# Kernel optimization log

Measured on AMD Instinct MI355X. Metric: run time of the kernel, lower is better.

Reference implementation:

```python
import jax, jax.numpy as jnp
import numpy as np
from jax import lax

B, NF, NOBJ, SZ = 16, 4, 32, 128
HALF = SZ // 2  # 64


def _build_grid(h, w):
    ys = jnp.linspace(0.0, 1.0, h)
    xs = jnp.linspace(0.0, 1.0, w)
    gy, gx = jnp.meshgrid(ys, xs, indexing='ij')
    g = jnp.stack([gy, gx], axis=-1)  # (H, W, 2)
    return jnp.concatenate([g, 1.0 - g], axis=-1)[None]  # (1, H, W, 4)


def setup_inputs() -> dict:
    key = jax.random.key(0)
    ks = jax.random.split(key, 8)
    images = jax.random.normal(ks[0], (B, 3 * NF, SZ, SZ), dtype=jnp.float32)
    rois = jax.random.randint(ks[1], (B, NOBJ, SZ, SZ), 0, 2).astype(jnp.bool_)
    conv1_w = jax.random.normal(ks[2], (64, 3 * NF, 3, 3), dtype=jnp.float32) * 0.05
    conv1_b = jnp.zeros((64,), dtype=jnp.float32)
    conv2_w = jax.random.normal(ks[3], (128, 64, 3, 3), dtype=jnp.float32) * 0.05
    conv2_b = jnp.zeros((128,), dtype=jnp.float32)
    dense_w = jax.random.normal(ks[4], (128, 4), dtype=jnp.float32) * 0.1
    dense_b = jnp.zeros((128,), dtype=jnp.float32)
    return dict(images=images, rois=rois, conv1_w=conv1_w, conv1_b=conv1_b,
                conv2_w=conv2_w, conv2_b=conv2_b, dense_w=dense_w, dense_b=dense_b)


def _conv(x, w, b):
    y = lax.conv_general_dilated(x, w, window_strides=(1, 1), padding='SAME',
                                 dimension_numbers=('NCHW', 'OIHW', 'NCHW'))
    return y + b[None, :, None, None]


def reference(images, rois, conv1_w, conv1_b, conv2_w, conv2_b, dense_w, dense_b):
    # conv stack
    x = jax.nn.relu(_conv(images, conv1_w, conv1_b))
    x = lax.reduce_window(x, -jnp.inf, lax.max, (1, 1, 2, 2), (1, 1, 2, 2), 'VALID')
    x = jax.nn.relu(_conv(x, conv2_w, conv2_b))  # (B, 128, 64, 64)
    # soft position embed
    grid = _build_grid(HALF, HALF)  # (1, 64, 64, 4)
    pe = grid @ dense_w.T + dense_b  # (1, 64, 64, 128)
    x = x + jnp.transpose(pe, (0, 3, 1, 2))  # (B, 128, 64, 64)
    # roi pool: nearest-downsample masks 128->64 (indices 0,2,4,...)
    r = rois[:, :, ::2, ::2].astype(x.dtype)  # (B, O, 64, 64)
    masked = x[:, None] * r[:, :, None]  # (B, O, 128, 64, 64)
    return jnp.max(masked, axis=(-2, -1))  # (B, O, 128)
```

## Files before the change

### kernel.cpp

```cpp
#include <hip/hip_runtime.h>


typedef __attribute__((ext_vector_type(8))) short short8;
typedef __attribute__((ext_vector_type(4))) float f32x4;
typedef __attribute__((ext_vector_type(4))) unsigned short us4;
typedef __attribute__((ext_vector_type(2))) unsigned short u16x2;
typedef unsigned short u16;
typedef unsigned int u32;

__device__ __forceinline__ u16 f2bf(float f) {
  u32 u = __builtin_bit_cast(u32, f);
  return (u16)((u + 0x7fffu + ((u >> 16) & 1u)) >> 16);
}
__device__ __forceinline__ u32 pkmaxu(u32 a, u32 b) {
  u16x2 x = __builtin_bit_cast(u16x2, a), y = __builtin_bit_cast(u16x2, b);
  return __builtin_bit_cast(u32, __builtin_elementwise_max(x, y));
}
__device__ __forceinline__ u32 map2(u32 v) {
  u32 flip = ((v & 0x80008000u) >> 15) * 0xFFFFu;
  return v ^ (flip | 0x80008000u);
}
__device__ __forceinline__ float unmap1(u32 m) {
  u32 b = m ^ ((m & 0x8000u) ? 0x8000u : 0xFFFFu);
  return __builtin_bit_cast(float, b << 16);
}

namespace {

__global__ __launch_bounds__(256) void kiop(const float* __restrict__ img,
                                            u16* __restrict__ imgT,
                                            const unsigned* __restrict__ rois,
                                            unsigned* __restrict__ rmask,
                                            const float* __restrict__ w2,
                                            u16* __restrict__ Aw2,
                                            const float* __restrict__ w1,
                                            u16* __restrict__ Aw1) {
  __shared__ alignas(16) u16 ST[2048];
  const int bx = blockIdx.x;
  const int t = threadIdx.x;
  if (bx < 2048) {
    const int row = bx & 127, b = bx >> 7;
#pragma unroll
    for (int i = 0; i < 2; ++i) {
      const int e = i * 256 + t;
      ST[(e >> 2) * 16 + 12 + (e & 3)] = 0;
    }
#pragma unroll
    for (int i = 0; i < 6; ++i) {
      const int e = i * 256 + t;
      const int ci = e >> 7, col = e & 127;
      const float v = img[(((size_t)(b * 12 + ci)) << 14) + row * 128 + col];
      ST[col * 16 + ci] = f2bf(v);
    }
    __syncthreads();
    us4* dst = (us4*)(imgT + (((size_t)(b * 128 + row)) << 11));
#pragma unroll
    for (int i = 0; i < 2; ++i) {
      const int q = i * 256 + t;
      dst[q] = *(const us4*)&ST[q * 4];
    }
  } else if (bx < 2176) {
    const int lane = t & 63;
    u32 ok = 1u;
#pragma unroll
    for (int i = 0; i < 4; ++i) {
      u32 v = rois[lane * 4 + i];
      ok &= ((v <= 1u) || (v == 0x3f800000u)) ? 1u : 0u;
    }
    const bool isWord = (__all((int)ok) != 0);
    const unsigned char* roisB = (const unsigned char*)rois;
    const int pi = (bx - 2048) * 256 + t;
    const int b = pi >> 11;
    const int pp = pi & 2047;
    const int h = pp >> 5;
    const int wp = pp & 31;
    const size_t base = (size_t)b * 32 * 16384 + (size_t)(2 * h) * 128 + 4 * wp;
    u32 m0 = 0, m1 = 0;
#pragma unroll
    for (int o = 0; o < 32; ++o) {
      const size_t idx = base + (size_t)o * 16384;
      if (isWord) {
        const uint4 q = *(const uint4*)&rois[idx];
        m0 |= (u32)(q.x != 0u) << o;
        m1 |= (u32)(q.z != 0u) << o;
      } else {
        const u32 q = *(const u32*)&roisB[idx];
        m0 |= (u32)((q & 0xffu) != 0u) << o;
        m1 |= (u32)((q & 0xff0000u) != 0u) << o;
      }
    }
    *(uint2*)&rmask[b * 4096 + h * 64 + wp * 2] = make_uint2(m0, m1);
  } else if (bx < 2464) {
    const int idx = (bx - 2176) * 256 + t;
    const int j = idx & 7;
    const int lane = (idx >> 3) & 63;
    const int t3 = idx >> 9;
    const int ks = t3 % 18, cot = t3 / 18;
    const int m = lane & 15, g = lane >> 4;
    const int co = cot * 16 + m;
    const int k = ks * 32 + g * 8 + j;
    const int rc = k >> 6, ci = k & 63;
    Aw2[idx] = f2bf(w2[co * 576 + ci * 9 + rc]);
  } else {
    const int idx = (bx - 2464) * 256 + t;
    const int j = idx & 7;
    const int lane = (idx >> 3) & 63;
    const int t3 = idx >> 9;
    const int ks = t3 % 5, cot = t3 / 5;
    const int m = lane & 15, g = lane >> 4;
    const int co = cot * 16 + m;
    const int k = ks * 32 + g * 8 + j;
    const int rc = k >> 4, cip = k & 15;
    const float v = (rc < 9 && cip < 12) ? w1[co * 108 + cip * 9 + rc] : 0.f;
    Aw1[idx] = f2bf(v);
  }
}

__global__ __launch_bounds__(256) void k1_mfma(const u16* __restrict__ imgT,
                                               const u16* __restrict__ Aw1,
                                               const float* __restrict__ b1,
                                               u16* __restrict__ pooledT) {
  __shared__ alignas(16) u16 SIMG[8192];
  __shared__ alignas(16) u16 PT[64 * 68];
  const int h2 = blockIdx.x, b = blockIdx.y;
  const int t = threadIdx.x, wv = t >> 6, l = t & 63;

#pragma unroll
  for (int i = 0; i < 4; ++i) {
    const int q = i * 256 + t;
    const int sr = q >> 8, off = q & 255;
    const int irow = 2 * h2 - 1 + sr;
    short8 v = {0, 0, 0, 0, 0, 0, 0, 0};
    if ((unsigned)irow < 128u)
      v = *(const short8*)(imgT + (((size_t)(b * 128 + irow)) << 11) + off * 8);
    *(short8*)((char*)SIMG + ((q * 16) ^ (((q >> 3) & 1) << 4))) = v;
  }
  __syncthreads();

  const int m16 = l & 15, g = l >> 4;
  const int colhalf = wv >> 1, cotbase = (wv & 1) * 2;
  const int cipb = (g & 1) * 16;
  f32x4 acc[2][8];
#pragma unroll
  for (int ct = 0; ct < 2; ++ct)
#pragma unroll
    for (int pt = 0; pt < 8; ++pt) acc[ct][pt] = (f32x4){0.f, 0.f, 0.f, 0.f};

  const u16* awb = Aw1 + (size_t)l * 8;
  const short8 z8 = {0, 0, 0, 0, 0, 0, 0, 0};

#pragma unroll
  for (int ks = 0; ks < 5; ++ks) {
    short8 a0 = *(const short8*)(awb + (cotbase * 5 + ks) * 512);
    short8 a1 = *(const short8*)(awb + ((cotbase + 1) * 5 + ks) * 512);
    const bool pz = (ks == 4) && (g >= 2);
    const int rc = pz ? 0 : (2 * ks + (g >> 1));
    const int rr = (rc * 11) >> 5;
    const int cc = rc - rr * 3;
    const int d = m16 - 1 + cc;
    const int sb = (d < 0) ? 1 : ((d >> 2) & 1);
    const int base = rr * 4096 + d * 32 + colhalf * 2048 + (cipb ^ (sb << 4));
    const bool killLo = (cc == 0) && (m16 == 0) && (colhalf == 0);
    const bool killHi = (cc == 2) && (m16 == 15) && (colhalf == 1);
#pragma unroll
    for (int pt = 0; pt < 8; ++pt) {
      const int r01 = pt >> 2, ct2 = pt & 3;
      short8 bv = *(const short8*)((const char*)SIMG + base + r01 * 4096 + ct2 * 512);
      bool kill = pz;
      if (ct2 == 0) kill = kill || killLo;
      if (ct2 == 3) kill = kill || killHi;
      if (kill) bv = z8;
      acc[0][pt] = __builtin_amdgcn_mfma_f32_16x16x32_bf16(a0, bv, acc[0][pt], 0, 0, 0);
      acc[1][pt] = __builtin_amdgcn_mfma_f32_16x16x32_bf16(a1, bv, acc[1][pt], 0, 0, 0);
    }
  }

#pragma unroll
  for (int ct = 0; ct < 2; ++ct) {
    const int cot = cotbase + ct;
#pragma unroll
    for (int r = 0; r < 4; ++r) {
      const int co = cot * 16 + g * 4 + r;
      const float bias = b1[co];
#pragma unroll
      for (int ct2 = 0; ct2 < 4; ++ct2) {
        float v0 = fmaxf(acc[ct][ct2][r] + bias, 0.f);
        float v1 = fmaxf(acc[ct][4 + ct2][r] + bias, 0.f);
        float vv = fmaxf(v0, v1);
        vv = fmaxf(vv, __shfl_xor(vv, 1, 64));
        if (!(m16 & 1)) {
          const int pw = colhalf * 32 + ct2 * 8 + (m16 >> 1);
          PT[pw * 68 + co] = f2bf(vv);
        }
      }
    }
  }
  __syncthreads();
  u16* dst = pooledT + (((size_t)(b * 64 + h2)) << 12);
#pragma unroll
  for (int i = 0; i < 4; ++i) {
    const int e = (i * 256 + t) * 4;
    const int pw = e >> 6, co = e & 63;
    *(us4*)(dst + e) = *(const us4*)&PT[pw * 68 + co];
  }
}

__global__ __launch_bounds__(256) void k2f(const u16* __restrict__ pooledT,
                                           const u16* __restrict__ Aw,
                                           const float* __restrict__ b2,
                                           const float* __restrict__ dw,
                                           const float* __restrict__ db,
                                           const unsigned* __restrict__ rmask,
                                           u32* __restrict__ partial) {
  __shared__ alignas(16) char SB[32768];
  __shared__ u32 MS[128];
  const int hp = blockIdx.x, b = blockIdx.y;
  const int t = threadIdx.x, wv = t >> 6, l = t & 63;

#pragma unroll
  for (int i = 0; i < 8; ++i) {
    const int chunk = i * 4 + wv;
    const int row = chunk >> 3;
    const int hin = 2 * hp - 1 + row;
    short8 v = {0, 0, 0, 0, 0, 0, 0, 0};
    if ((unsigned)hin < 64u)
      v = *(const short8*)(pooledT + (((size_t)(b * 64 + hin)) << 12) +
                           ((chunk & 7) << 9) + l * 8);
    const int lin = chunk * 1024 + l * 16;
    *(short8*)(SB + (lin ^ (((lin >> 7) & 7) << 4))) = v;
  }
  if (t < 128) MS[t] = rmask[b * 4096 + hp * 128 + t];
  __syncthreads();

  const int m16 = l & 15, g = l >> 4;
  const int kbyte = g * 16;
  f32x4 acc[2][8];
#pragma unroll
  for (int ct = 0; ct < 2; ++ct)
#pragma unroll
    for (int n = 0; n < 8; ++n) acc[ct][n] = (f32x4){0.f, 0.f, 0.f, 0.f};

  const u16* aw0 = Aw + (size_t)wv * 36 * 512 + l * 8;
  const short8 z8 = {0, 0, 0, 0, 0, 0, 0, 0};

#pragma unroll
  for (int ks = 0; ks < 18; ++ks) {
    const int rc = ks >> 1, r = rc / 3, c = rc % 3;
    const int koff = r * 8192 + (ks & 1) * 64 + kbyte;
    short8 a0 = *(const short8*)(aw0 + ks * 512);
    short8 a1 = *(const short8*)(aw0 + (18 + ks) * 512);
    const int d = m16 + c - 1;
    const int base = (koff + d * 128) ^ ((d & 7) << 4);
    const bool edgeLo = (c == 0) && (m16 == 0);
    const bool edgeHi = (c == 2) && (m16 == 15);
#pragma unroll
    for (int n = 0; n < 8; ++n) {
      const int orw = n >> 2, n4 = n & 3;
      short8 bv = *(const short8*)(SB + base + orw * 8192 + n4 * 2048);
      if (c == 0 && n4 == 0) { if (edgeLo) bv = z8; }
      if (c == 2 && n4 == 3) { if (edgeHi) bv = z8; }
      acc[0][n] = __builtin_amdgcn_mfma_f32_16x16x32_bf16(a0, bv, acc[0][n], 0, 0, 0);
      acc[1][n] = __builtin_amdgcn_mfma_f32_16x16x32_bf16(a1, bv, acc[1][n], 0, 0, 0);
    }
  }

  __syncthreads();

  const float inv63 = 1.f / 63.f;
#pragma unroll
  for (int ct = 0; ct < 2; ++ct) {
    const int cot = wv * 2 + ct;
#pragma unroll
    for (int r2 = 0; r2 < 2; ++r2) {
      const int co0 = cot * 16 + g * 4 + r2 * 2;
      const float bias0 = b2[co0], bias1 = b2[co0 + 1];
      const float pA0 = dw[co0 * 4 + 0] - dw[co0 * 4 + 2];
      const float pB0 = dw[co0 * 4 + 1] - dw[co0 * 4 + 3];
      const float pC0 = dw[co0 * 4 + 2] + dw[co0 * 4 + 3] + db[co0];
      const float pA1 = dw[co0 * 4 + 4] - dw[co0 * 4 + 6];
      const float pB1 = dw[co0 * 4 + 5] - dw[co0 * 4 + 7];
      const float pC1 = dw[co0 * 4 + 6] + dw[co0 * 4 + 7] + db[co0 + 1];
#pragma unroll
      for (int orw = 0; orw < 2; ++orw) {
        const float gy = (float)(2 * hp + orw) * inv63;
        const float pe00 = gy * pA0 + pC0;
        const float pe01 = gy * pA1 + pC1;
#pragma unroll
        for (int n4 = 0; n4 < 4; ++n4) {
          const int w = n4 * 16 + m16;
          const int pos = orw * 64 + w;
          const float gx = (float)w * inv63;
          const float v0 = fmaxf(acc[ct][orw * 4 + n4][r2 * 2 + 0] + bias0, 0.f)
                           + pe00 + gx * pB0;
          const float v1 = fmaxf(acc[ct][orw * 4 + n4][r2 * 2 + 1] + bias1, 0.f)
                           + pe01 + gx * pB1;
          const u32 pk = map2((u32)f2bf(v0) | ((u32)f2bf(v1) << 16));
          *(u32*)(SB + ((pos * 256 + co0 * 2) ^ ((pos & 7) << 4))) = pk;
        }
      }
    }
  }
  __syncthreads();

  const int og = t >> 5, coq = t & 31;
  u32 a0[4], a1[4];
#pragma unroll
  for (int r = 0; r < 4; ++r) { a0[r] = 0x80008000u; a1[r] = 0x80008000u; }
  for (int pos = 0; pos < 128; ++pos) {
    const u32 mw = MS[pos];
    const uint2 x = *(const uint2*)(SB + ((pos * 256 + coq * 8) ^ ((pos & 7) << 4)));
#pragma unroll
    for (int r = 0; r < 4; ++r) {
      const int o = og * 4 + r;
      const u32 am = (u32)((int)(mw << (31 - o)) >> 31);
      a0[r] = pkmaxu(a0[r], x.x & am);
      a1[r] = pkmaxu(a1[r], x.y & am);
    }
  }
  u32* pslab = partial + (size_t)hp * 32768;
#pragma unroll
  for (int r = 0; r < 4; ++r) {
    const int o = og * 4 + r;
    *(uint2*)&pslab[((b * 32 + o) << 6) + coq * 2] = make_uint2(a0[r], a1[r]);
  }
}

__global__ __launch_bounds__(256) void k4_merge(const u32* __restrict__ partial,
                                                float* __restrict__ out) {
  const int idx = blockIdx.x * 256 + threadIdx.x;
  u32 v = partial[idx];
#pragma unroll
  for (int q = 1; q < 32; ++q) v = pkmaxu(v, partial[q * 32768 + idx]);
  float2 o2;
  o2.x = unmap1(v & 0xFFFFu);
  o2.y = unmap1(v >> 16);
  *(float2*)&out[idx * 2] = o2;
}

}

extern "C" void kernel_launch(void* const* d_in, const int* in_sizes, int n_in,
                              void* d_out, int out_size, void* d_ws, size_t ws_size,
                              hipStream_t stream) {
  const float* images = (const float*)d_in[0];
  const unsigned* rois = (const unsigned*)d_in[1];
  const float* w1 = (const float*)d_in[2];
  const float* b1 = (const float*)d_in[3];
  const float* w2 = (const float*)d_in[4];
  const float* b2 = (const float*)d_in[5];
  const float* dw = (const float*)d_in[6];
  const float* db = (const float*)d_in[7];
  float* out = (float*)d_out;

  char* ws = (char*)d_ws;
  unsigned* rmask = (unsigned*)(ws);
  u16* pooledT = (u16*)(ws + 0x40000);
  u16* Aw2 = (u16*)(ws + 0x840000);
  u16* Aw1 = (u16*)(ws + 0x864000);
  u16* imgT = (u16*)(ws + 0x900000);
  u32* partial = (u32*)(ws + 0xD00000);

  hipLaunchKernelGGL(kiop, dim3(2504), dim3(256), 0, stream,
                     images, imgT, rois, rmask, w2, Aw2, w1, Aw1);
  hipLaunchKernelGGL(k1_mfma, dim3(64, 16), dim3(256), 0, stream, imgT, Aw1, b1, pooledT);
  hipLaunchKernelGGL(k2f, dim3(32, 16), dim3(256), 0, stream,
                     pooledT, Aw2, b2, dw, db, rmask, partial);
  hipLaunchKernelGGL(k4_merge, dim3(128), dim3(256), 0, stream, partial, out);
}
```

Baseline: 61.64 us.

## Move roi-mask and conv2 weight prep into conv1 kernel; halve conv2 rows per block

The roi bitmask build and the conv2 weight repack move out of the first prep kernel and run as extra blocks of the conv1 MFMA kernel, which now uses a flat 1D grid. The aim is to overlap these side tasks with conv1 compute instead of serialising them before it. The conv2+pool kernel now covers one output row per block instead of two, doubling the grid to 1024 blocks and cutting LDS and accumulator registers for better occupancy. The cost is more halo reloads of pooled input and weight loads across blocks, plus 64 partial slabs for the merge kernel to reduce instead of 32.

```diff
diff --git a/kernel.cpp b/kernel.cpp
--- a/kernel.cpp
+++ b/kernel.cpp
@@ -29,10 +29,6 @@
 
 __global__ __launch_bounds__(256) void kiop(const float* __restrict__ img,
                                             u16* __restrict__ imgT,
-                                            const unsigned* __restrict__ rois,
-                                            unsigned* __restrict__ rmask,
-                                            const float* __restrict__ w2,
-                                            u16* __restrict__ Aw2,
                                             const float* __restrict__ w1,
                                             u16* __restrict__ Aw1) {
   __shared__ alignas(16) u16 ST[2048];
@@ -59,50 +55,8 @@
       const int q = i * 256 + t;
       dst[q] = *(const us4*)&ST[q * 4];
     }
-  } else if (bx < 2176) {
-    const int lane = t & 63;
-    u32 ok = 1u;
-#pragma unroll
-    for (int i = 0; i < 4; ++i) {
-      u32 v = rois[lane * 4 + i];
-      ok &= ((v <= 1u) || (v == 0x3f800000u)) ? 1u : 0u;
-    }
-    const bool isWord = (__all((int)ok) != 0);
-    const unsigned char* roisB = (const unsigned char*)rois;
-    const int pi = (bx - 2048) * 256 + t;
-    const int b = pi >> 11;
-    const int pp = pi & 2047;
-    const int h = pp >> 5;
-    const int wp = pp & 31;
-    const size_t base = (size_t)b * 32 * 16384 + (size_t)(2 * h) * 128 + 4 * wp;
-    u32 m0 = 0, m1 = 0;
-#pragma unroll
-    for (int o = 0; o < 32; ++o) {
-      const size_t idx = base + (size_t)o * 16384;
-      if (isWord) {
-        const uint4 q = *(const uint4*)&rois[idx];
-        m0 |= (u32)(q.x != 0u) << o;
-        m1 |= (u32)(q.z != 0u) << o;
-      } else {
-        const u32 q = *(const u32*)&roisB[idx];
-        m0 |= (u32)((q & 0xffu) != 0u) << o;
-        m1 |= (u32)((q & 0xff0000u) != 0u) << o;
-      }
-    }
-    *(uint2*)&rmask[b * 4096 + h * 64 + wp * 2] = make_uint2(m0, m1);
-  } else if (bx < 2464) {
-    const int idx = (bx - 2176) * 256 + t;
-    const int j = idx & 7;
-    const int lane = (idx >> 3) & 63;
-    const int t3 = idx >> 9;
-    const int ks = t3 % 18, cot = t3 / 18;
-    const int m = lane & 15, g = lane >> 4;
-    const int co = cot * 16 + m;
-    const int k = ks * 32 + g * 8 + j;
-    const int rc = k >> 6, ci = k & 63;
-    Aw2[idx] = f2bf(w2[co * 576 + ci * 9 + rc]);
   } else {
-    const int idx = (bx - 2464) * 256 + t;
+    const int idx = (bx - 2048) * 256 + t;
     const int j = idx & 7;
     const int lane = (idx >> 3) & 63;
     const int t3 = idx >> 9;
@@ -119,11 +73,65 @@
 __global__ __launch_bounds__(256) void k1_mfma(const u16* __restrict__ imgT,
                                                const u16* __restrict__ Aw1,
                                                const float* __restrict__ b1,
-                                               u16* __restrict__ pooledT) {
+                                               u16* __restrict__ pooledT,
+                                               const float* __restrict__ w2,
+                                               u16* __restrict__ Aw2,
+                                               const unsigned* __restrict__ rois,
+                                               unsigned* __restrict__ rmask) {
   __shared__ alignas(16) u16 SIMG[8192];
   __shared__ alignas(16) u16 PT[64 * 68];
-  const int h2 = blockIdx.x, b = blockIdx.y;
-  const int t = threadIdx.x, wv = t >> 6, l = t & 63;
+  const int bx = blockIdx.x;
+  const int t = threadIdx.x;
+
+  if (bx >= 1024) {
+    if (bx < 1312) {
+      const int idx = (bx - 1024) * 256 + t;
+      const int j = idx & 7;
+      const int lane = (idx >> 3) & 63;
+      const int t3 = idx >> 9;
+      const int ks = t3 % 18, cot = t3 / 18;
+      const int m = lane & 15, g = lane >> 4;
+      const int co = cot * 16 + m;
+      const int k = ks * 32 + g * 8 + j;
+      const int rc = k >> 6, ci = k & 63;
+      Aw2[idx] = f2bf(w2[co * 576 + ci * 9 + rc]);
+    } else {
+      const int lane = t & 63;
+      u32 ok = 1u;
+#pragma unroll
+      for (int i = 0; i < 4; ++i) {
+        u32 v = rois[lane * 4 + i];
+        ok &= ((v <= 1u) || (v == 0x3f800000u)) ? 1u : 0u;
+      }
+      const bool isWord = (__all((int)ok) != 0);
+      const unsigned char* roisB = (const unsigned char*)rois;
+      const int pi = (bx - 1312) * 256 + t;
+      const int b = pi >> 11;
+      const int pp = pi & 2047;
+      const int h = pp >> 5;
+      const int wp = pp & 31;
+      const size_t base = (size_t)b * 32 * 16384 + (size_t)(2 * h) * 128 + 4 * wp;
+      u32 m0 = 0, m1 = 0;
+#pragma unroll
+      for (int o = 0; o < 32; ++o) {
+        const size_t idx = base + (size_t)o * 16384;
+        if (isWord) {
+          const uint4 q = *(const uint4*)&rois[idx];
+          m0 |= (u32)(q.x != 0u) << o;
+          m1 |= (u32)(q.z != 0u) << o;
+        } else {
+          const u32 q = *(const u32*)&roisB[idx];
+          m0 |= (u32)((q & 0xffu) != 0u) << o;
+          m1 |= (u32)((q & 0xff0000u) != 0u) << o;
+        }
+      }
+      *(uint2*)&rmask[b * 4096 + h * 64 + wp * 2] = make_uint2(m0, m1);
+    }
+    return;
+  }
+
+  const int h2 = bx & 63, b = bx >> 6;
+  const int wv = t >> 6, l = t & 63;
 
 #pragma unroll
   for (int i = 0; i < 4; ++i) {
@@ -212,16 +220,16 @@
                                            const float* __restrict__ db,
                                            const unsigned* __restrict__ rmask,
                                            u32* __restrict__ partial) {
-  __shared__ alignas(16) char SB[32768];
-  __shared__ u32 MS[128];
-  const int hp = blockIdx.x, b = blockIdx.y;
+  __shared__ alignas(16) char SB[25088];
+  __shared__ u32 MS[64];
+  const int h = blockIdx.x, b = blockIdx.y;
   const int t = threadIdx.x, wv = t >> 6, l = t & 63;
 
 #pragma unroll
-  for (int i = 0; i < 8; ++i) {
+  for (int i = 0; i < 6; ++i) {
     const int chunk = i * 4 + wv;
     const int row = chunk >> 3;
-    const int hin = 2 * hp - 1 + row;
+    const int hin = h - 1 + row;
     short8 v = {0, 0, 0, 0, 0, 0, 0, 0};
     if ((unsigned)hin < 64u)
       v = *(const short8*)(pooledT + (((size_t)(b * 64 + hin)) << 12) +
@@ -229,16 +237,16 @@
     const int lin = chunk * 1024 + l * 16;
     *(short8*)(SB + (lin ^ (((lin >> 7) & 7) << 4))) = v;
   }
-  if (t < 128) MS[t] = rmask[b * 4096 + hp * 128 + t];
+  if (t < 64) MS[t] = rmask[b * 4096 + h * 64 + t];
   __syncthreads();
 
   const int m16 = l & 15, g = l >> 4;
   const int kbyte = g * 16;
-  f32x4 acc[2][8];
+  f32x4 acc[2][4];
 #pragma unroll
   for (int ct = 0; ct < 2; ++ct)
 #pragma unroll
-    for (int n = 0; n < 8; ++n) acc[ct][n] = (f32x4){0.f, 0.f, 0.f, 0.f};
+    for (int n = 0; n < 4; ++n) acc[ct][n] = (f32x4){0.f, 0.f, 0.f, 0.f};
 
   const u16* aw0 = Aw + (size_t)wv * 36 * 512 + l * 8;
   const short8 z8 = {0, 0, 0, 0, 0, 0, 0, 0};
@@ -254,11 +262,10 @@
     const bool edgeLo = (c == 0) && (m16 == 0);
     const bool edgeHi = (c == 2) && (m16 == 15);
 #pragma unroll
-    for (int n = 0; n < 8; ++n) {
-      const int orw = n >> 2, n4 = n & 3;
-      short8 bv = *(const short8*)(SB + base + orw * 8192 + n4 * 2048);
-      if (c == 0 && n4 == 0) { if (edgeLo) bv = z8; }
-      if (c == 2 && n4 == 3) { if (edgeHi) bv = z8; }
+    for (int n = 0; n < 4; ++n) {
+      short8 bv = *(const short8*)(SB + base + n * 2048);
+      if (c == 0 && n == 0) { if (edgeLo) bv = z8; }
+      if (c == 2 && n == 3) { if (edgeHi) bv = z8; }
       acc[0][n] = __builtin_amdgcn_mfma_f32_16x16x32_bf16(a0, bv, acc[0][n], 0, 0, 0);
       acc[1][n] = __builtin_amdgcn_mfma_f32_16x16x32_bf16(a1, bv, acc[1][n], 0, 0, 0);
     }
@@ -267,6 +274,7 @@
   __syncthreads();
 
   const float inv63 = 1.f / 63.f;
+  const float gy = (float)h * inv63;
 #pragma unroll
   for (int ct = 0; ct < 2; ++ct) {
     const int cot = wv * 2 + ct;
@@ -280,23 +288,16 @@
       const float pA1 = dw[co0 * 4 + 4] - dw[co0 * 4 + 6];
       const float pB1 = dw[co0 * 4 + 5] - dw[co0 * 4 + 7];
       const float pC1 = dw[co0 * 4 + 6] + dw[co0 * 4 + 7] + db[co0 + 1];
-#pragma unroll
-      for (int orw = 0; orw < 2; ++orw) {
-        const float gy = (float)(2 * hp + orw) * inv63;
-        const float pe00 = gy * pA0 + pC0;
-        const float pe01 = gy * pA1 + pC1;
-#pragma unroll
-        for (int n4 = 0; n4 < 4; ++n4) {
-          const int w = n4 * 16 + m16;
-          const int pos = orw * 64 + w;
-          const float gx = (float)w * inv63;
-          const float v0 = fmaxf(acc[ct][orw * 4 + n4][r2 * 2 + 0] + bias0, 0.f)
-                           + pe00 + gx * pB0;
-          const float v1 = fmaxf(acc[ct][orw * 4 + n4][r2 * 2 + 1] + bias1, 0.f)
-                           + pe01 + gx * pB1;
-          const u32 pk = map2((u32)f2bf(v0) | ((u32)f2bf(v1) << 16));
-          *(u32*)(SB + ((pos * 256 + co0 * 2) ^ ((pos & 7) << 4))) = pk;
-        }
+      const float pe00 = gy * pA0 + pC0;
+      const float pe01 = gy * pA1 + pC1;
+#pragma unroll
+      for (int n4 = 0; n4 < 4; ++n4) {
+        const int w = n4 * 16 + m16;
+        const float gx = (float)w * inv63;
+        const float v0 = fmaxf(acc[ct][n4][r2 * 2 + 0] + bias0, 0.f) + pe00 + gx * pB0;
+        const float v1 = fmaxf(acc[ct][n4][r2 * 2 + 1] + bias1, 0.f) + pe01 + gx * pB1;
+        const u32 pk = map2((u32)f2bf(v0) | ((u32)f2bf(v1) << 16));
+        *(u32*)(SB + ((w * 256 + co0 * 2) ^ ((w & 7) << 4))) = pk;
       }
     }
   }
@@ -306,7 +307,7 @@
   u32 a0[4], a1[4];
 #pragma unroll
   for (int r = 0; r < 4; ++r) { a0[r] = 0x80008000u; a1[r] = 0x80008000u; }
-  for (int pos = 0; pos < 128; ++pos) {
+  for (int pos = 0; pos < 64; ++pos) {
     const u32 mw = MS[pos];
     const uint2 x = *(const uint2*)(SB + ((pos * 256 + coq * 8) ^ ((pos & 7) << 4)));
 #pragma unroll
@@ -317,7 +318,7 @@
       a1[r] = pkmaxu(a1[r], x.y & am);
     }
   }
-  u32* pslab = partial + (size_t)hp * 32768;
+  u32* pslab = partial + (size_t)h * 32768;
 #pragma unroll
   for (int r = 0; r < 4; ++r) {
     const int o = og * 4 + r;
@@ -330,7 +331,7 @@
   const int idx = blockIdx.x * 256 + threadIdx.x;
   u32 v = partial[idx];
 #pragma unroll
-  for (int q = 1; q < 32; ++q) v = pkmaxu(v, partial[q * 32768 + idx]);
+  for (int q = 1; q < 64; ++q) v = pkmaxu(v, partial[q * 32768 + idx]);
   float2 o2;
   o2.x = unmap1(v & 0xFFFFu);
   o2.y = unmap1(v >> 16);
@@ -360,10 +361,11 @@
   u16* imgT = (u16*)(ws + 0x900000);
   u32* partial = (u32*)(ws + 0xD00000);
 
-  hipLaunchKernelGGL(kiop, dim3(2504), dim3(256), 0, stream,
-                     images, imgT, rois, rmask, w2, Aw2, w1, Aw1);
-  hipLaunchKernelGGL(k1_mfma, dim3(64, 16), dim3(256), 0, stream, imgT, Aw1, b1, pooledT);
-  hipLaunchKernelGGL(k2f, dim3(32, 16), dim3(256), 0, stream,
+  hipLaunchKernelGGL(kiop, dim3(2088), dim3(256), 0, stream,
+                     images, imgT, w1, Aw1);
+  hipLaunchKernelGGL(k1_mfma, dim3(1440), dim3(256), 0, stream,
+                     imgT, Aw1, b1, pooledT, w2, Aw2, rois, rmask);
+  hipLaunchKernelGGL(k2f, dim3(64, 16), dim3(256), 0, stream,
                      pooledT, Aw2, b2, dw, db, rmask, partial);
   hipLaunchKernelGGL(k4_merge, dim3(128), dim3(256), 0, stream, partial, out);
 }
```

Measured after the change: 73.17 us. 1.19x slower.
